# Kernel tuning notes

Hardware: AMD Instinct MI355X
Metric: run time of the kernel (lower is better)

## Reference

```python
import jax, jax.numpy as jnp
import numpy as np

MASK_VAL = -1e9

def setup_inputs() -> dict:
    key = jax.random.key(0)
    kq, kk, kv, km = jax.random.split(key, 4)
    bz, lq, lk, d = 16, 2048, 2048, 64
    q = jax.random.normal(kq, (bz, lq, d), dtype=jnp.float32)
    k = jax.random.normal(kk, (bz, lk, d), dtype=jnp.float32)
    v = jax.random.normal(kv, (bz, lk, d), dtype=jnp.float32)
    # pad mask: True = masked-out position
    pad_mask = jax.random.randint(km, (bz, lq, lk), 0, 2) == 1
    return {"q": q, "k": k, "v": v, "pad_mask": pad_mask}

def reference(q, k, v, pad_mask):
    # scores: [bz, lq, lk]
    d = k.shape[-1]
    scores = jnp.einsum('bqd,bkd->bqk', q, k) / jnp.sqrt(jnp.asarray(d, q.dtype))
    scores = jnp.where(pad_mask, jnp.asarray(MASK_VAL, scores.dtype), scores)
    attn = jax.nn.softmax(scores, axis=-1)  # dropout inactive in eval mode
    out = jnp.einsum('bqk,bkd->bqd', attn, v)
    return out
```

## Files before the change

kernel.cpp:

```cpp
#include <hip/hip_runtime.h>
#include <hip/hip_bf16.h>
#include <cstdint>
#include <cstddef>

typedef __attribute__((ext_vector_type(8))) short  short8;
typedef __attribute__((ext_vector_type(4))) short  short4v;
typedef __attribute__((ext_vector_type(4))) float  f32x4;
typedef __attribute__((ext_vector_type(4))) int    i32x4;

#define BZ   16
#define LQ   2048
#define LK   2048
#define DD   64
#define QBLK 64
#define KVB  64
#define NIT  (LK / KVB)

__global__ __launch_bounds__(256)
void pack_mask(const int* __restrict__ m, uint32_t* __restrict__ out) {
    size_t t = (size_t)blockIdx.x * 256 + threadIdx.x;
    const i32x4* p = reinterpret_cast<const i32x4*>(m + t * 32);
    uint32_t w = 0;
    #pragma unroll
    for (int j = 0; j < 8; ++j) {
        i32x4 v = p[j];
        w |= (v.x != 0 ? 1u : 0u) << (j * 4 + 0);
        w |= (v.y != 0 ? 1u : 0u) << (j * 4 + 1);
        w |= (v.z != 0 ? 1u : 0u) << (j * 4 + 2);
        w |= (v.w != 0 ? 1u : 0u) << (j * 4 + 3);
    }
    out[t] = w;
}

__device__ inline short bfs(float f) {
    __hip_bfloat16 h = __float2bfloat16(f);
    union { __hip_bfloat16 h; short s; } u; u.h = h; return u.s;
}

template<int CTRL>
__device__ inline float dppf(float x) {
    return __int_as_float(__builtin_amdgcn_update_dpp(0, __float_as_int(x), CTRL, 0xF, 0xF, false));
}
__device__ inline float rmax16(float x) {
    x = fmaxf(x, dppf<0xB1>(x));
    x = fmaxf(x, dppf<0x4E>(x));
    x = fmaxf(x, dppf<0x124>(x));
    x = fmaxf(x, dppf<0x128>(x));
    return x;
}
__device__ inline float rsum16(float x) {
    x += dppf<0xB1>(x);
    x += dppf<0x4E>(x);
    x += dppf<0x124>(x);
    x += dppf<0x128>(x);
    return x;
}

__device__ inline void glds16(const float* gp, void* lp) {
    __builtin_amdgcn_global_load_lds(
        (const __attribute__((address_space(1))) void*)(gp),
        (__attribute__((address_space(3))) void*)(lp),
        16, 0, 0);
}

__global__ __launch_bounds__(256, 2)
void attn_fwd(const float* __restrict__ Qg, const float* __restrict__ Kg,
              const float* __restrict__ Vg, const uint32_t* __restrict__ MW,
              float* __restrict__ Og)
{
    __shared__ alignas(128) float Kbuf[2][KVB * DD];
    __shared__ alignas(128) float Vbuf[2][KVB * DD];
    __shared__ alignas(128) short PQ[4][16 * 64];

    const int t = threadIdx.x;
    const int w = t >> 6;
    const int l = t & 63;
    const int g = l >> 4;
    const int n = l & 15;

    const int nb   = blockIdx.x;
    const int xcd  = nb & 7;
    const int jj   = nb >> 3;
    const int b    = xcd + 8 * (jj >> 5);
    const int qtl  = jj & 31;
    const int qbase = qtl * QBLK;

    const float* Qb = Qg + ((size_t)b * LQ + qbase) * DD;
    const float* Kb = Kg + (size_t)b * LK * DD;
    const float* Vb = Vg + (size_t)b * LK * DD;
    const uint32_t* mwp = MW + ((size_t)b * LQ + qbase) * 64;

    auto stage = [&](int it, int sel) {
        #pragma unroll
        for (int s = 0; s < 4; ++s) {
            int CH  = s * 4 + w;
            int kv  = CH * 4 + g;
            int psw = (kv & 7) ^ (kv >> 3);
            size_t go = (size_t)(it * KVB + kv) * DD + (size_t)((((n >> 1) ^ psw) * 8) + (n & 1) * 4);
            glds16(Kb + go, (void*)&Kbuf[sel][CH * 256]);
            glds16(Vb + go, (void*)&Vbuf[sel][CH * 256]);
        }
    };

    stage(0, 0);
    {
        int qr = t >> 2;
        int db = (t & 3) * 16;
        short* row = &PQ[qr >> 4][(qr & 15) * 64];
        #pragma unroll
        for (int k2 = 0; k2 < 4; ++k2) {
            f32x4 qv = *(const f32x4*)(Qb + (size_t)qr * DD + db + k2 * 4);
            int dd = db + k2 * 4;
            short4v qp;
            qp.x = bfs(qv.x); qp.y = bfs(qv.y); qp.z = bfs(qv.z); qp.w = bfs(qv.w);
            *(short4v*)((char*)row + ((dd * 2) ^ ((qr & 7) << 4))) = qp;
        }
    }
    __syncthreads();

    short8 aQ[2];
    {
        short* row = &PQ[w][n * 64];
        #pragma unroll
        for (int s = 0; s < 2; ++s)
            aQ[s] = *(short8*)((char*)row + ((s * 64 + g * 16) ^ ((n & 7) << 4)));
    }

    f32x4 Oacc[4];
    #pragma unroll
    for (int c = 0; c < 4; ++c) { Oacc[c].x = 0.f; Oacc[c].y = 0.f; Oacc[c].z = 0.f; Oacc[c].w = 0.f; }
    float m2[4]   = { -1e30f, -1e30f, -1e30f, -1e30f };
    float lsum[4] = { 0.f, 0.f, 0.f, 0.f };

    const float SC2 = 0.125f * 1.4426950408889634f;
    short* Pw = &PQ[w][0];

    for (int it = 0; it < NIT; ++it) {
        const int cur = it & 1;
        if (it + 1 < NIT) stage(it + 1, cur ^ 1);

        uint32_t mw0[4], mw1[4];
        #pragma unroll
        for (int r = 0; r < 4; ++r) {
            uint2 v = *(const uint2*)(mwp + (size_t)(w * 16 + g * 4 + r) * 64 + it * 2);
            mw0[r] = v.x; mw1[r] = v.y;
        }

        f32x4 S[4];
        #pragma unroll
        for (int c = 0; c < 4; ++c) { S[c].x = 0.f; S[c].y = 0.f; S[c].z = 0.f; S[c].w = 0.f; }
        __builtin_amdgcn_s_setprio(1);
        #pragma unroll
        for (int c = 0; c < 4; ++c) {
            int kvl = c * 16 + n;
            int psw = (kvl & 7) ^ (kvl >> 3);
            #pragma unroll
            for (int s = 0; s < 2; ++s) {
                const char* bp = (const char*)&Kbuf[cur][kvl * 64] + (((s * 4 + g) ^ psw) * 32);
                f32x4 h0 = *(const f32x4*)bp;
                f32x4 h1 = *(const f32x4*)(bp + 16);
                short8 bk;
                bk[0] = bfs(h0.x); bk[1] = bfs(h0.y); bk[2] = bfs(h0.z); bk[3] = bfs(h0.w);
                bk[4] = bfs(h1.x); bk[5] = bfs(h1.y); bk[6] = bfs(h1.z); bk[7] = bfs(h1.w);
                S[c] = __builtin_amdgcn_mfma_f32_16x16x32_bf16(aQ[s], bk, S[c], 0, 0, 0);
            }
        }
        __builtin_amdgcn_s_setprio(0);

        #pragma unroll
        for (int c = 0; c < 4; ++c)
            #pragma unroll
            for (int r = 0; r < 4; ++r) {
                uint32_t mword = (c & 2) ? mw1[r] : mw0[r];
                uint32_t bit = (mword >> ((c & 1) * 16 + n)) & 1u;
                float x = S[c][r] * SC2;
                S[c][r] = bit ? -1.0e9f : x;
            }

        #pragma unroll
        for (int r = 0; r < 4; ++r) {
            float mx = fmaxf(fmaxf(S[0][r], S[1][r]), fmaxf(S[2][r], S[3][r]));
            mx = rmax16(mx);
            float mnew = fmaxf(m2[r], mx);
            float resc = exp2f(m2[r] - mnew);
            m2[r] = mnew;
            lsum[r] *= resc;
            #pragma unroll
            for (int c = 0; c < 4; ++c) Oacc[c][r] *= resc;

            float rs = 0.f;
            int q_ = g * 4 + r;
            #pragma unroll
            for (int c = 0; c < 4; ++c) {
                float p = exp2f(S[c][r] - mnew);
                rs += p;
                *((short*)((char*)Pw + q_ * 128 + (((c * 16 + n) * 2) ^ ((q_ & 7) << 4)))) = bfs(p);
            }
            lsum[r] += rsum16(rs);
        }

        __builtin_amdgcn_s_setprio(1);
        #pragma unroll
        for (int ks = 0; ks < 2; ++ks) {
            short8 aP = *(short8*)((char*)Pw + n * 128 + ((ks * 64 + g * 16) ^ ((n & 7) << 4)));
            #pragma unroll
            for (int c = 0; c < 4; ++c) {
                float ve[8];
                #pragma unroll
                for (int e = 0; e < 8; ++e) {
                    int kve = ks * 32 + g * 8 + e;
                    int pswv = e ^ (ks * 4 + g);
                    const char* p = (const char*)&Vbuf[cur][kve * 64]
                                  + ((((c * 2) + (n >> 3)) ^ pswv) * 32)
                                  + ((n >> 2) & 1) * 16 + (n & 3) * 4;
                    ve[e] = *(const float*)p;
                }
                short8 bv;
                bv[0] = bfs(ve[0]); bv[1] = bfs(ve[1]); bv[2] = bfs(ve[2]); bv[3] = bfs(ve[3]);
                bv[4] = bfs(ve[4]); bv[5] = bfs(ve[5]); bv[6] = bfs(ve[6]); bv[7] = bfs(ve[7]);
                Oacc[c] = __builtin_amdgcn_mfma_f32_16x16x32_bf16(aP, bv, Oacc[c], 0, 0, 0);
            }
        }
        __builtin_amdgcn_s_setprio(0);

        __syncthreads();
    }

    #pragma unroll
    for (int r = 0; r < 4; ++r) {
        float inv = 1.0f / lsum[r];
        #pragma unroll
        for (int c = 0; c < 4; ++c)
            Og[((size_t)b * LQ + qbase + w * 16 + g * 4 + r) * DD + c * 16 + n] = Oacc[c][r] * inv;
    }
}

extern "C" void kernel_launch(void* const* d_in, const int* in_sizes, int n_in,
                              void* d_out, int out_size, void* d_ws, size_t ws_size,
                              hipStream_t stream) {
    const float* q = (const float*)d_in[0];
    const float* k = (const float*)d_in[1];
    const float* v = (const float*)d_in[2];
    const int*   m = (const int*)d_in[3];
    float* out = (float*)d_out;
    uint32_t* mw = (uint32_t*)d_ws;

    pack_mask<<<dim3((BZ * LQ * (LK / 32)) / 256), dim3(256), 0, stream>>>(m, mw);
    attn_fwd<<<dim3(BZ * (LQ / QBLK)), dim3(256), 0, stream>>>(q, k, v, mw, out);
}
```

Baseline: 475.3 us.

## Pre-convert K/V to swizzled bf16 tiles and read mask directly in attention

Adds a prep kernel that converts K to bf16 and V to transposed bf16, both in swizzled 64x64 tiles. The attention kernel can then stage half the bytes into LDS and feed MFMA operands with single 16-byte LDS reads instead of per-element float loads and conversions. The separate mask-packing kernel is removed: each thread loads its raw int mask values one iteration ahead and builds the bits in registers. Synchronisation is restructured around s_barrier plus an explicit vmcnt wait. The trade-off is that the raw 256 MB int mask is now read inside the attention loop with scattered 4-byte loads, and a manual round-to-nearest bf16 conversion replaces the library call.

Result: faster. 401.1 us (-15.6%).

```diff
diff --git a/kernel.cpp b/kernel.cpp
--- a/kernel.cpp
+++ b/kernel.cpp
@@ -6,7 +6,6 @@
 typedef __attribute__((ext_vector_type(8))) short  short8;
 typedef __attribute__((ext_vector_type(4))) short  short4v;
 typedef __attribute__((ext_vector_type(4))) float  f32x4;
-typedef __attribute__((ext_vector_type(4))) int    i32x4;
 
 #define BZ   16
 #define LQ   2048
@@ -16,25 +15,10 @@
 #define KVB  64
 #define NIT  (LK / KVB)
 
-__global__ __launch_bounds__(256)
-void pack_mask(const int* __restrict__ m, uint32_t* __restrict__ out) {
-    size_t t = (size_t)blockIdx.x * 256 + threadIdx.x;
-    const i32x4* p = reinterpret_cast<const i32x4*>(m + t * 32);
-    uint32_t w = 0;
-    #pragma unroll
-    for (int j = 0; j < 8; ++j) {
-        i32x4 v = p[j];
-        w |= (v.x != 0 ? 1u : 0u) << (j * 4 + 0);
-        w |= (v.y != 0 ? 1u : 0u) << (j * 4 + 1);
-        w |= (v.z != 0 ? 1u : 0u) << (j * 4 + 2);
-        w |= (v.w != 0 ? 1u : 0u) << (j * 4 + 3);
-    }
-    out[t] = w;
-}
-
 __device__ inline short bfs(float f) {
-    __hip_bfloat16 h = __float2bfloat16(f);
-    union { __hip_bfloat16 h; short s; } u; u.h = h; return u.s;
+    union { float f; uint32_t u; } x; x.f = f;
+    uint32_t r = x.u + 0x7fffu + ((x.u >> 16) & 1u);
+    return (short)(r >> 16);
 }
 
 template<int CTRL>
@@ -56,74 +40,123 @@
     return x;
 }
 
-__device__ inline void glds16(const float* gp, void* lp) {
+__device__ inline void glds16(const void* gp, void* lp) {
     __builtin_amdgcn_global_load_lds(
-        (const __attribute__((address_space(1))) void*)(gp),
-        (__attribute__((address_space(3))) void*)(lp),
-        16, 0, 0);
+        (const __attribute__((address_space(1))) void*)gp,
+        (__attribute__((address_space(3))) void*)lp, 16, 0, 0);
+}
+
+__global__ __launch_bounds__(256)
+void prep_kv(const float* __restrict__ K, const float* __restrict__ V,
+             short* __restrict__ Ko, short* __restrict__ Vo)
+{
+    __shared__ float T[64 * 65];
+    const int blk = blockIdx.x;
+    const int t = threadIdx.x;
+    const int row = t >> 2;
+    const int c4  = (t & 3) * 16;
+    const float* Ks = K + (size_t)blk * 4096;
+    const float* Vs = V + (size_t)blk * 4096;
+    char* Kt = (char*)Ko + (size_t)blk * 8192;
+    char* Vt = (char*)Vo + (size_t)blk * 8192;
+
+    #pragma unroll
+    for (int h = 0; h < 2; ++h) {
+        f32x4 a = *(const f32x4*)(Ks + row * 64 + c4 + h * 8);
+        f32x4 b = *(const f32x4*)(Ks + row * 64 + c4 + h * 8 + 4);
+        short8 o;
+        o[0] = bfs(a.x); o[1] = bfs(a.y); o[2] = bfs(a.z); o[3] = bfs(a.w);
+        o[4] = bfs(b.x); o[5] = bfs(b.y); o[6] = bfs(b.z); o[7] = bfs(b.w);
+        int gr = (c4 >> 3) + h;
+        *(short8*)(Kt + row * 128 + ((gr ^ (row & 7)) * 16)) = o;
+    }
+    #pragma unroll
+    for (int j = 0; j < 4; ++j) {
+        f32x4 v4 = *(const f32x4*)(Vs + row * 64 + c4 + j * 4);
+        T[row * 65 + c4 + j * 4 + 0] = v4.x;
+        T[row * 65 + c4 + j * 4 + 1] = v4.y;
+        T[row * 65 + c4 + j * 4 + 2] = v4.z;
+        T[row * 65 + c4 + j * 4 + 3] = v4.w;
+    }
+    __syncthreads();
+    #pragma unroll
+    for (int h = 0; h < 2; ++h) {
+        short8 o;
+        #pragma unroll
+        for (int e = 0; e < 8; ++e)
+            o[e] = bfs(T[(c4 + h * 8 + e) * 65 + row]);
+        int gr = (c4 >> 3) + h;
+        *(short8*)(Vt + row * 128 + ((gr ^ (row & 7)) * 16)) = o;
+    }
 }
 
 __global__ __launch_bounds__(256, 2)
-void attn_fwd(const float* __restrict__ Qg, const float* __restrict__ Kg,
-              const float* __restrict__ Vg, const uint32_t* __restrict__ MW,
+void attn_fwd(const float* __restrict__ Qg, const short* __restrict__ Ko,
+              const short* __restrict__ Vo, const int* __restrict__ Mg,
               float* __restrict__ Og)
 {
-    __shared__ alignas(128) float Kbuf[2][KVB * DD];
-    __shared__ alignas(128) float Vbuf[2][KVB * DD];
+    __shared__ alignas(128) short Kbuf[2][KVB * DD];
+    __shared__ alignas(128) short Vbuf[2][KVB * DD];
     __shared__ alignas(128) short PQ[4][16 * 64];
 
     const int t = threadIdx.x;
-    const int w = t >> 6;
-    const int l = t & 63;
-    const int g = l >> 4;
-    const int n = l & 15;
-
-    const int nb   = blockIdx.x;
-    const int xcd  = nb & 7;
-    const int jj   = nb >> 3;
-    const int b    = xcd + 8 * (jj >> 5);
-    const int qtl  = jj & 31;
-    const int qbase = qtl * QBLK;
+    const int w = t >> 6, l = t & 63, g = l >> 4, n = l & 15;
+
+    const int nb = blockIdx.x, xcd = nb & 7, jj = nb >> 3;
+    const int b = xcd + 8 * (jj >> 5), qtl = jj & 31, qbase = qtl * QBLK;
 
     const float* Qb = Qg + ((size_t)b * LQ + qbase) * DD;
-    const float* Kb = Kg + (size_t)b * LK * DD;
-    const float* Vb = Vg + (size_t)b * LK * DD;
-    const uint32_t* mwp = MW + ((size_t)b * LQ + qbase) * 64;
-
-    auto stage = [&](int it, int sel) {
-        #pragma unroll
-        for (int s = 0; s < 4; ++s) {
-            int CH  = s * 4 + w;
-            int kv  = CH * 4 + g;
-            int psw = (kv & 7) ^ (kv >> 3);
-            size_t go = (size_t)(it * KVB + kv) * DD + (size_t)((((n >> 1) ^ psw) * 8) + (n & 1) * 4);
-            glds16(Kb + go, (void*)&Kbuf[sel][CH * 256]);
-            glds16(Vb + go, (void*)&Vbuf[sel][CH * 256]);
+    const char* Ktiles = (const char*)Ko + (size_t)b * 32 * 8192;
+    const char* Vtiles = (const char*)Vo + (size_t)b * 32 * 8192;
+    const int*  mbase  = Mg + ((size_t)b * LQ + qbase + w * 16 + g * 4) * (size_t)LK + n;
+
+    auto stage = [&](int it2, int sel) {
+        const char* ksrc = Ktiles + (size_t)it2 * 8192;
+        const char* vsrc = Vtiles + (size_t)it2 * 8192;
+        #pragma unroll
+        for (int j2 = 0; j2 < 2; ++j2) {
+            int ch = w * 2 + j2;
+            glds16(ksrc + ch * 1024 + l * 16, (char*)&Kbuf[sel][0] + ch * 1024);
+            glds16(vsrc + ch * 1024 + l * 16, (char*)&Vbuf[sel][0] + ch * 1024);
         }
     };
 
+    int mv[16];
+    auto mload = [&](int it2) {
+        #pragma unroll
+        for (int r = 0; r < 4; ++r)
+            #pragma unroll
+            for (int c = 0; c < 4; ++c)
+                mv[r * 4 + c] = mbase[(size_t)r * LK + it2 * 64 + c * 16];
+    };
+
+    const int qr = t >> 2, db = (t & 3) * 16;
+    f32x4 q0[4];
+    #pragma unroll
+    for (int k2 = 0; k2 < 4; ++k2)
+        q0[k2] = *(const f32x4*)(Qb + (size_t)qr * DD + db + k2 * 4);
+
     stage(0, 0);
+    mload(0);
+    asm volatile("" ::: "memory");
+
     {
-        int qr = t >> 2;
-        int db = (t & 3) * 16;
-        short* row = &PQ[qr >> 4][(qr & 15) * 64];
+        short* rowp = &PQ[qr >> 4][(qr & 15) * 64];
         #pragma unroll
         for (int k2 = 0; k2 < 4; ++k2) {
-            f32x4 qv = *(const f32x4*)(Qb + (size_t)qr * DD + db + k2 * 4);
             int dd = db + k2 * 4;
             short4v qp;
-            qp.x = bfs(qv.x); qp.y = bfs(qv.y); qp.z = bfs(qv.z); qp.w = bfs(qv.w);
-            *(short4v*)((char*)row + ((dd * 2) ^ ((qr & 7) << 4))) = qp;
-        }
-    }
-    __syncthreads();
-
+            qp.x = bfs(q0[k2].x); qp.y = bfs(q0[k2].y);
+            qp.z = bfs(q0[k2].z); qp.w = bfs(q0[k2].w);
+            *(short4v*)((char*)rowp + ((dd * 2) ^ ((qr & 7) << 4))) = qp;
+        }
+    }
     short8 aQ[2];
     {
-        short* row = &PQ[w][n * 64];
-        #pragma unroll
-        for (int s = 0; s < 2; ++s)
-            aQ[s] = *(short8*)((char*)row + ((s * 64 + g * 16) ^ ((n & 7) << 4)));
+        short* rowp = &PQ[w][n * 64];
+        #pragma unroll
+        for (int s2 = 0; s2 < 2; ++s2)
+            aQ[s2] = *(short8*)((char*)rowp + ((s2 * 64 + g * 16) ^ ((n & 7) << 4)));
     }
 
     f32x4 Oacc[4];
@@ -131,20 +164,26 @@
     for (int c = 0; c < 4; ++c) { Oacc[c].x = 0.f; Oacc[c].y = 0.f; Oacc[c].z = 0.f; Oacc[c].w = 0.f; }
     float m2[4]   = { -1e30f, -1e30f, -1e30f, -1e30f };
     float lsum[4] = { 0.f, 0.f, 0.f, 0.f };
-
     const float SC2 = 0.125f * 1.4426950408889634f;
     short* Pw = &PQ[w][0];
 
     for (int it = 0; it < NIT; ++it) {
         const int cur = it & 1;
-        if (it + 1 < NIT) stage(it + 1, cur ^ 1);
-
-        uint32_t mw0[4], mw1[4];
-        #pragma unroll
-        for (int r = 0; r < 4; ++r) {
-            uint2 v = *(const uint2*)(mwp + (size_t)(w * 16 + g * 4 + r) * 64 + it * 2);
-            mw0[r] = v.x; mw1[r] = v.y;
-        }
+        __builtin_amdgcn_s_barrier();
+        asm volatile("s_waitcnt vmcnt(0)" ::: "memory");
+        __builtin_amdgcn_sched_barrier(0);
+
+        uint32_t mbits = 0;
+        #pragma unroll
+        for (int i = 0; i < 16; ++i) mbits |= (mv[i] != 0) ? (1u << i) : 0u;
+
+        const int nx = (it + 1 < NIT) ? it + 1 : NIT - 1;
+        stage(nx, cur ^ 1);
+        mload(nx);
+        asm volatile("" ::: "memory");
+
+        const char* Kc = (const char*)&Kbuf[cur][0];
+        const char* Vc = (const char*)&Vbuf[cur][0];
 
         f32x4 S[4];
         #pragma unroll
@@ -153,16 +192,10 @@
         #pragma unroll
         for (int c = 0; c < 4; ++c) {
             int kvl = c * 16 + n;
-            int psw = (kvl & 7) ^ (kvl >> 3);
-            #pragma unroll
-            for (int s = 0; s < 2; ++s) {
-                const char* bp = (const char*)&Kbuf[cur][kvl * 64] + (((s * 4 + g) ^ psw) * 32);
-                f32x4 h0 = *(const f32x4*)bp;
-                f32x4 h1 = *(const f32x4*)(bp + 16);
-                short8 bk;
-                bk[0] = bfs(h0.x); bk[1] = bfs(h0.y); bk[2] = bfs(h0.z); bk[3] = bfs(h0.w);
-                bk[4] = bfs(h1.x); bk[5] = bfs(h1.y); bk[6] = bfs(h1.z); bk[7] = bfs(h1.w);
-                S[c] = __builtin_amdgcn_mfma_f32_16x16x32_bf16(aQ[s], bk, S[c], 0, 0, 0);
+            #pragma unroll
+            for (int s2 = 0; s2 < 2; ++s2) {
+                short8 bk = *(const short8*)(Kc + kvl * 128 + (((s2 * 4 + g) ^ (kvl & 7)) * 16));
+                S[c] = __builtin_amdgcn_mfma_f32_16x16x32_bf16(aQ[s2], bk, S[c], 0, 0, 0);
             }
         }
         __builtin_amdgcn_s_setprio(0);
@@ -171,10 +204,8 @@
         for (int c = 0; c < 4; ++c)
             #pragma unroll
             for (int r = 0; r < 4; ++r) {
-                uint32_t mword = (c & 2) ? mw1[r] : mw0[r];
-                uint32_t bit = (mword >> ((c & 1) * 16 + n)) & 1u;
                 float x = S[c][r] * SC2;
-                S[c][r] = bit ? -1.0e9f : x;
+                S[c][r] = ((mbits >> (r * 4 + c)) & 1u) ? -1.0e9f : x;
             }
 
         #pragma unroll
@@ -205,27 +236,15 @@
             short8 aP = *(short8*)((char*)Pw + n * 128 + ((ks * 64 + g * 16) ^ ((n & 7) << 4)));
             #pragma unroll
             for (int c = 0; c < 4; ++c) {
-                float ve[8];
-                #pragma unroll
-                for (int e = 0; e < 8; ++e) {
-                    int kve = ks * 32 + g * 8 + e;
-                    int pswv = e ^ (ks * 4 + g);
-                    const char* p = (const char*)&Vbuf[cur][kve * 64]
-                                  + ((((c * 2) + (n >> 3)) ^ pswv) * 32)
-                                  + ((n >> 2) & 1) * 16 + (n & 3) * 4;
-                    ve[e] = *(const float*)p;
-                }
-                short8 bv;
-                bv[0] = bfs(ve[0]); bv[1] = bfs(ve[1]); bv[2] = bfs(ve[2]); bv[3] = bfs(ve[3]);
-                bv[4] = bfs(ve[4]); bv[5] = bfs(ve[5]); bv[6] = bfs(ve[6]); bv[7] = bfs(ve[7]);
+                int d = c * 16 + n;
+                short8 bv = *(const short8*)(Vc + d * 128 + (((ks * 4 + g) ^ (d & 7)) * 16));
                 Oacc[c] = __builtin_amdgcn_mfma_f32_16x16x32_bf16(aP, bv, Oacc[c], 0, 0, 0);
             }
         }
         __builtin_amdgcn_s_setprio(0);
-
-        __syncthreads();
-    }
-
+    }
+
+    asm volatile("s_waitcnt vmcnt(0)" ::: "memory");
     #pragma unroll
     for (int r = 0; r < 4; ++r) {
         float inv = 1.0f / lsum[r];
@@ -243,8 +262,9 @@
     const float* v = (const float*)d_in[2];
     const int*   m = (const int*)d_in[3];
     float* out = (float*)d_out;
-    uint32_t* mw = (uint32_t*)d_ws;
-
-    pack_mask<<<dim3((BZ * LQ * (LK / 32)) / 256), dim3(256), 0, stream>>>(m, mw);
-    attn_fwd<<<dim3(BZ * (LQ / QBLK)), dim3(256), 0, stream>>>(q, k, v, mw, out);
-}
+    short* Ko = (short*)d_ws;
+    short* Vo = (short*)((char*)d_ws + (4u << 20));
+
+    prep_kv<<<dim3(BZ * (LK / KVB)), dim3(256), 0, stream>>>(k, v, Ko, Vo);
+    attn_fwd<<<dim3(BZ * (LQ / QBLK)), dim3(256), 0, stream>>>(q, Ko, Vo, m, out);
+}
```
